# Kernel optimization log

Hardware: AMD Instinct MI355X
Metric: run time of the kernel (lower is better)

The kernel has to match this reference:

```python
import jax, jax.numpy as jnp
import numpy as np

B, H, W, C = 4, 48, 48, 256
NUM_HEADS = 8
DEPTH = C // NUM_HEADS  # 32


def setup_inputs() -> dict:
    key = jax.random.key(0)
    ks = jax.random.split(key, 8)
    scale = 1.0 / np.sqrt(C)
    return {
        "inputs": jax.random.normal(ks[0], (B, H, W, C), dtype=jnp.float32),
        "wq": jax.random.normal(ks[1], (C, C), dtype=jnp.float32) * scale,
        "bq": jax.random.normal(ks[2], (C,), dtype=jnp.float32) * 0.01,
        "wk": jax.random.normal(ks[3], (C, C), dtype=jnp.float32) * scale,
        "bk": jax.random.normal(ks[4], (C,), dtype=jnp.float32) * 0.01,
        "wv": jax.random.normal(ks[5], (C, C), dtype=jnp.float32) * scale,
        "bv": jax.random.normal(ks[6], (C,), dtype=jnp.float32) * 0.01,
        "gamma": jax.random.normal(ks[7], (), dtype=jnp.float32) * 0.1,
    }


def reference(inputs, wq, bq, wk, bk, wv, bv, gamma):
    b, h, w, c = inputs.shape
    n = h * w  # number of tokens

    def proj_split(wm, bm):
        # 1x1 conv == per-pixel dense: [b,h,w,c] @ [c,c] + bias
        y = jnp.einsum('bhwc,cd->bhwd', inputs, wm) + bm
        # split heads -> [b, num_heads, n, depth]
        return y.reshape(b, n, NUM_HEADS, DEPTH).transpose(0, 2, 1, 3)

    q = proj_split(wq, bq) / jnp.sqrt(jnp.asarray(DEPTH, inputs.dtype))
    k = proj_split(wk, bk)
    v = proj_split(wv, bv)

    s = jnp.einsum('bnqd,bnkd->bnqk', q, k)        # [b, heads, n, n]
    a = jax.nn.softmax(s, axis=-1)
    o = jnp.einsum('bnqk,bnkd->bnqd', a, v)        # [b, heads, n, depth]
    o = o.transpose(0, 2, 1, 3).reshape(b, h, w, c)
    return gamma * o + inputs
```

## Files before the change

kernel.cpp:

```cpp
#include <hip/hip_runtime.h>
#include <hip/hip_bf16.h>
#include <cstdint>

#define B_    4
#define NH    8
#define N_TOK 2304
#define D_    32
#define C_    256
#define M_ROWS (B_ * N_TOK)
#define KVB   128
#define NT2   (N_TOK / KVB)
#define M_FIX 10.0f

typedef float  f32x4  __attribute__((ext_vector_type(4)));
typedef short  bf16x8 __attribute__((ext_vector_type(8)));

#define GLOADLDS(g, l) __builtin_amdgcn_global_load_lds( \
    (const __attribute__((address_space(1))) unsigned*)(g), \
    (__attribute__((address_space(3))) unsigned*)(l), 16, 0, 0)

static __device__ __forceinline__ unsigned short f2bf(float f) {
    union { float f; unsigned u; } v; v.f = f;
    unsigned u = v.u;
    u += 0x7FFF + ((u >> 16) & 1);
    return (unsigned short)(u >> 16);
}

static __device__ __forceinline__ unsigned cvt_pk_bf16(float a, float b) {
    unsigned r;
    asm("v_cvt_pk_bf16_f32 %0, %1, %2" : "=v"(r) : "v"(a), "v"(b));
    return r;
}

__global__ void k_prep_x(const float* __restrict__ x, unsigned short* __restrict__ xb) {
    int i = blockIdx.x * blockDim.x + threadIdx.x;
    float4 v = reinterpret_cast<const float4*>(x)[i];
    ushort4 o;
    o.x = f2bf(v.x); o.y = f2bf(v.y); o.z = f2bf(v.z); o.w = f2bf(v.w);
    reinterpret_cast<ushort4*>(xb)[i] = o;
}

__global__ void k_prep_w(const float* __restrict__ w0, const float* __restrict__ w1,
                         const float* __restrict__ w2, unsigned short* __restrict__ wt) {
    __shared__ float tile[64][65];
    int mat = blockIdx.y;
    const float* w = (mat == 0) ? w0 : (mat == 1) ? w1 : w2;
    int t   = blockIdx.x;
    int tc  = (t & 3) * 64;
    int td  = (t >> 2) * 64;
    int tid = threadIdx.x;
    int r0  = tid >> 6;
    int x0  = tid & 63;
#pragma unroll
    for (int it = 0; it < 16; ++it) {
        int c = it * 4 + r0;
        tile[c][x0] = w[(tc + c) * C_ + td + x0];
    }
    __syncthreads();
    unsigned short* wto = wt + mat * (C_ * C_);
#pragma unroll
    for (int it = 0; it < 16; ++it) {
        int d = it * 4 + r0;
        wto[(td + d) * C_ + tc + x0] = f2bf(tile[x0][d]);
    }
}

__global__ __launch_bounds__(256) void k_proj(
    const unsigned short* __restrict__ xb,
    const unsigned short* __restrict__ wtb,
    const float* __restrict__ bq, const float* __restrict__ bk, const float* __restrict__ bv,
    unsigned short* __restrict__ qo, unsigned short* __restrict__ ko, unsigned short* __restrict__ vto)
{
    __shared__ __align__(16) unsigned short A_lds[2][64][32];
    __shared__ __align__(16) unsigned short B_lds[2][128][32];

    int rows0 = blockIdx.x * 64;
    int cols0 = blockIdx.y * 128;
    int mat   = cols0 >> 8;
    const float* bias = (mat == 0) ? bq : (mat == 1) ? bk : bv;
    float scale = (mat == 0) ? (0.17677669529663687f * 1.4426950408889634f) : 1.0f;

    int tid = threadIdx.x, wave = tid >> 6, lane = tid & 63;
    int lr = lane & 15, lg = lane >> 4;
    int wr = wave >> 1, wc = wave & 1;

    int srow = lane >> 2, sslot = lane & 3;
    int ra   = wave * 16 + srow;
    int keyA = ((ra >> 1) & 1) | (((ra >> 3) & 1) << 1);
    const unsigned short* asrc = xb + (rows0 + ra) * C_ + ((sslot ^ keyA) * 8);
    int rb   = wave * 32 + srow;
    int keyB0 = ((rb >> 1) & 1) | (((rb >> 3) & 1) << 1);
    int keyB1 = (((rb + 16) >> 1) & 1) | ((((rb + 16) >> 3) & 1) << 1);
    const unsigned short* bsrc0 = wtb + (cols0 + rb) * C_ + ((sslot ^ keyB0) * 8);
    const unsigned short* bsrc1 = wtb + (cols0 + rb + 16) * C_ + ((sslot ^ keyB1) * 8);

    char* aldsb = (char*)&A_lds[0][0][0];
    char* bldsb = (char*)&B_lds[0][0][0];
    int adst = wave * 1024;
    int bdst0 = wave * 2048, bdst1 = bdst0 + 1024;

    int xorb = (((lr >> 1) & 1) << 4) | (((lr >> 3) & 1) << 5);
    int fcol = (lg * 16) ^ xorb;
    int arow0 = wr * 32 + lr;
    int brow0 = wc * 64 + lr;

    GLOADLDS(asrc, aldsb + adst);
    GLOADLDS(bsrc0, bldsb + bdst0);
    GLOADLDS(bsrc1, bldsb + bdst1);
    __syncthreads();

    f32x4 acc[2][4];
#pragma unroll
    for (int i = 0; i < 2; ++i)
#pragma unroll
        for (int j = 0; j < 4; ++j) acc[i][j] = (f32x4){0.f, 0.f, 0.f, 0.f};

    int buf = 0;
    for (int ks = 0; ks < 8; ++ks) {
        if (ks < 7) {
            int ko_ = (ks + 1) * 32;
            char* ad = aldsb + (buf ^ 1) * 4096;
            char* bd = bldsb + (buf ^ 1) * 8192;
            GLOADLDS(asrc + ko_, ad + adst);
            GLOADLDS(bsrc0 + ko_, bd + bdst0);
            GLOADLDS(bsrc1 + ko_, bd + bdst1);
        }
        const char* ac = aldsb + buf * 4096;
        const char* bc = bldsb + buf * 8192;

        bf16x8 a[2], b[4];
#pragma unroll
        for (int fr = 0; fr < 2; ++fr)
            a[fr] = *reinterpret_cast<const bf16x8*>(ac + (arow0 + fr * 16) * 64 + fcol);
#pragma unroll
        for (int fn = 0; fn < 4; ++fn)
            b[fn] = *reinterpret_cast<const bf16x8*>(bc + (brow0 + fn * 16) * 64 + fcol);

        __builtin_amdgcn_s_setprio(1);
#pragma unroll
        for (int fr = 0; fr < 2; ++fr)
#pragma unroll
            for (int fn = 0; fn < 4; ++fn)
                acc[fr][fn] = __builtin_amdgcn_mfma_f32_16x16x32_bf16(a[fr], b[fn], acc[fr][fn], 0, 0, 0);
        __builtin_amdgcn_s_setprio(0);

        __syncthreads();
        buf ^= 1;
    }

    int bidx = rows0 / N_TOK;
    int nb   = rows0 - bidx * N_TOK + wr * 32 + lg * 4;

    if (mat == 2) {
#pragma unroll
        for (int fr = 0; fr < 2; ++fr)
#pragma unroll
            for (int fn = 0; fn < 4; ++fn) {
                int cm = (cols0 & 255) + wc * 64 + fn * 16 + lr;
                float bsv = bias[cm];
                int hh = cm >> 5, d = cm & 31;
                uint2 pr;
                pr.x = cvt_pk_bf16(acc[fr][fn][0] + bsv, acc[fr][fn][1] + bsv);
                pr.y = cvt_pk_bf16(acc[fr][fn][2] + bsv, acc[fr][fn][3] + bsv);
                *reinterpret_cast<uint2*>(vto + ((bidx * NH + hh) * D_ + d) * N_TOK + nb + fr * 16) = pr;
            }
    } else {
        unsigned short* dst = (mat == 0) ? qo : ko;
#pragma unroll
        for (int fr = 0; fr < 2; ++fr)
#pragma unroll
            for (int fn = 0; fn < 4; ++fn) {
                int cm = (cols0 & 255) + wc * 64 + fn * 16 + lr;
                float bsv = bias[cm];
                int hh = cm >> 5, d = cm & 31;
#pragma unroll
                for (int j = 0; j < 4; ++j) {
                    float val = (acc[fr][fn][j] + bsv) * scale;
                    dst[((bidx * NH + hh) * N_TOK + nb + fr * 16 + j) * D_ + d] = f2bf(val);
                }
            }
    }
}

__global__ __launch_bounds__(512, 4) void k_attn(
    const unsigned short* __restrict__ qb,
    const unsigned short* __restrict__ kb,
    const unsigned short* __restrict__ vtg,
    const float* __restrict__ x,
    const float* __restrict__ gamma_p,
    float* __restrict__ out)
{
    __shared__ __align__(16) unsigned short K_lds[3][KVB][32];
    __shared__ __align__(16) unsigned short Vt_lds[3][32][KVB];

    int wid = (blockIdx.x & 7) * 72 + (blockIdx.x >> 3);
    int bh  = wid / 18;
    int qb0 = (wid % 18) * 128;

    int tid = threadIdx.x, wave = tid >> 6, lane = tid & 63;
    int lr = lane & 15, lg = lane >> 4;

    const unsigned short* Q  = qb  + bh * N_TOK * D_;
    const unsigned short* K  = kb  + bh * N_TOK * D_;
    const unsigned short* Vt = vtg + bh * D_ * N_TOK;

    int qrow = qb0 + wave * 16 + lr;
    bf16x8 q_frag = *reinterpret_cast<const bf16x8*>(Q + qrow * D_ + lg * 8);

    bool stK = wave < 4;
    int  sw  = stK ? wave : (wave - 4);
    int c0   = sw * 2;
    int kr0  = 32 * sw + (lane >> 2);
    int kslot = ((kr0 >> 1) & 1) | (((kr0 >> 3) & 1) << 1);
    int koff0 = kr0 * D_ + (((lane & 3) ^ kslot) * 8);
    int koff1 = koff0 + 16 * D_;
    int vr0   = 8 * sw + (lane >> 4);
    int voff0 = vr0 * N_TOK + (((lane & 15) ^ (vr0 & 7)) * 8);
    int voff1 = (vr0 + 4) * N_TOK + (((lane & 15) ^ ((vr0 + 4) & 7)) * 8);

    char* kldsb = (char*)&K_lds[0][0][0];
    char* vldsb = (char*)&Vt_lds[0][0][0];
    int dst0 = c0 * 1024, dst1 = dst0 + 1024;

#define STAGE(st, bidx) do {                                    \
        if (stK) {                                              \
            const unsigned short* Kn = K + (st) * (KVB * D_);   \
            char* kd = kldsb + (bidx) * 8192;                   \
            GLOADLDS(Kn + koff0, kd + dst0);                    \
            GLOADLDS(Kn + koff1, kd + dst1);                    \
        } else {                                                \
            const unsigned short* Vn = Vt + (st) * KVB;         \
            char* vd = vldsb + (bidx) * 8192;                   \
            GLOADLDS(Vn + voff0, vd + dst0);                    \
            GLOADLDS(Vn + voff1, vd + dst1);                    \
        } } while (0)

    STAGE(0, 0);
    STAGE(1, 1);
    asm volatile("s_waitcnt vmcnt(2)" ::: "memory");
    __builtin_amdgcn_s_barrier();

    f32x4 acc0  = (f32x4){0.f, 0.f, 0.f, 0.f};
    f32x4 acc1  = (f32x4){0.f, 0.f, 0.f, 0.f};
    f32x4 acc_l = (f32x4){0.f, 0.f, 0.f, 0.f};

    union { unsigned w[4]; bf16x8 v; } ones;
    ones.w[0] = 0x3F803F80u; ones.w[1] = 0x3F803F80u;
    ones.w[2] = 0x3F803F80u; ones.w[3] = 0x3F803F80u;

    int kread_key = (((lr >> 1) & 1) << 4) | (((lr >> 2) & 1) << 5);
    int krow_lane = (8 * (lr >> 2) + (lr & 3)) * 64 + ((lg * 16) ^ kread_key);
    int vkey = (lr & 7) << 4;

    const f32x4 zinit = (f32x4){-M_FIX, -M_FIX, -M_FIX, -M_FIX};

    int b0 = 0;
    for (int t = 0; t < NT2; ++t) {
        if (t + 2 < NT2) {
            int b2 = b0 + 2; if (b2 >= 3) b2 -= 3;
            STAGE(t + 2, b2);
        }
        const char* kc = kldsb + b0 * 8192;
        const char* vc = vldsb + b0 * 8192;

        f32x4 s[8];
        __builtin_amdgcn_s_setprio(1);
#pragma unroll
        for (int kt = 0; kt < 8; ++kt) {
            bf16x8 kf = *reinterpret_cast<const bf16x8*>(
                kc + (kt >> 1) * 2048 + (kt & 1) * 256 + krow_lane);
            s[kt] = __builtin_amdgcn_mfma_f32_16x16x32_bf16(kf, q_frag, zinit, 0, 0, 0);
        }
        __builtin_amdgcn_s_setprio(0);

#pragma unroll
        for (int kseg = 0; kseg < 4; ++kseg) {
            float e0 = __builtin_amdgcn_exp2f(s[2 * kseg][0]);
            float e1 = __builtin_amdgcn_exp2f(s[2 * kseg][1]);
            float e2 = __builtin_amdgcn_exp2f(s[2 * kseg][2]);
            float e3 = __builtin_amdgcn_exp2f(s[2 * kseg][3]);
            float e4 = __builtin_amdgcn_exp2f(s[2 * kseg + 1][0]);
            float e5 = __builtin_amdgcn_exp2f(s[2 * kseg + 1][1]);
            float e6 = __builtin_amdgcn_exp2f(s[2 * kseg + 1][2]);
            float e7 = __builtin_amdgcn_exp2f(s[2 * kseg + 1][3]);
            union { unsigned w[4]; bf16x8 v; } pa;
            pa.w[0] = cvt_pk_bf16(e0, e1);
            pa.w[1] = cvt_pk_bf16(e2, e3);
            pa.w[2] = cvt_pk_bf16(e4, e5);
            pa.w[3] = cvt_pk_bf16(e6, e7);
            int off = (kseg * 64 + lg * 16) ^ vkey;
            bf16x8 vf0 = *reinterpret_cast<const bf16x8*>(vc + lr * 256 + off);
            bf16x8 vf1 = *reinterpret_cast<const bf16x8*>(vc + (16 + lr) * 256 + off);
            acc0  = __builtin_amdgcn_mfma_f32_16x16x32_bf16(pa.v, vf0,    acc0,  0, 0, 0);
            acc1  = __builtin_amdgcn_mfma_f32_16x16x32_bf16(pa.v, vf1,    acc1,  0, 0, 0);
            acc_l = __builtin_amdgcn_mfma_f32_16x16x32_bf16(pa.v, ones.v, acc_l, 0, 0, 0);
        }

        if (t < NT2 - 1) {
            if (t + 2 < NT2) asm volatile("s_waitcnt vmcnt(2)" ::: "memory");
            else             asm volatile("s_waitcnt vmcnt(0)" ::: "memory");
            __builtin_amdgcn_s_barrier();
        }
        b0 = (b0 + 1 == 3) ? 0 : b0 + 1;
    }
#undef STAGE

    float g = gamma_p[0];
    int b = bh >> 3, head = bh & 7;
#pragma unroll
    for (int j = 0; j < 4; ++j) {
        float linv = 1.0f / acc_l[j];
        int n = qb0 + wave * 16 + 4 * lg + j;
        long r = (long)(b * N_TOK + n) * C_ + head * 32;
        out[r + lr]      = g * (acc0[j] * linv) + x[r + lr];
        out[r + 16 + lr] = g * (acc1[j] * linv) + x[r + 16 + lr];
    }
}

extern "C" void kernel_launch(void* const* d_in, const int* in_sizes, int n_in,
                              void* d_out, int out_size, void* d_ws, size_t ws_size,
                              hipStream_t stream) {
    const float* x     = (const float*)d_in[0];
    const float* wq    = (const float*)d_in[1];
    const float* bq    = (const float*)d_in[2];
    const float* wk    = (const float*)d_in[3];
    const float* bk    = (const float*)d_in[4];
    const float* wv    = (const float*)d_in[5];
    const float* bv    = (const float*)d_in[6];
    const float* gamma = (const float*)d_in[7];
    float* out = (float*)d_out;

    char* ws = (char*)d_ws;
    unsigned short* xb   = (unsigned short*)(ws);
    unsigned short* wt   = (unsigned short*)(ws + 4718592);
    unsigned short* qbuf = (unsigned short*)(ws + 5111808);
    unsigned short* kbuf = (unsigned short*)(ws + 9830400);
    unsigned short* vtg  = (unsigned short*)(ws + 14548992);

    k_prep_x<<<dim3(M_ROWS * C_ / 1024), dim3(256), 0, stream>>>(x, xb);
    k_prep_w<<<dim3(16, 3), dim3(256), 0, stream>>>(wq, wk, wv, wt);
    k_proj<<<dim3(M_ROWS / 64, 6), dim3(256), 0, stream>>>(xb, wt, bq, bk, bv, qbuf, kbuf, vtg);
    k_attn<<<dim3(N_TOK / 128 * B_ * NH), dim3(512), 0, stream>>>(qbuf, kbuf, vtg, x, gamma, out);
}
```

Measured before the change: 62.81 us.

## Triple-buffer projection GEMM loads and shrink attention blocks to six waves

The projection kernel moves from double to triple-buffered LDS staging, prefetching two k-steps ahead and using explicit vmcnt waits instead of a full syncthreads. The attention kernel now uses 384-thread blocks covering 96 query rows instead of 128. Four waves stage K and two waves stage V with four loads each, and the grid grows to 768 blocks. The aim is better latency hiding in the GEMM and better CU load balance in attention. The cost is more LDS per projection block and more redundant K/V loads per query row.

```diff
diff --git a/kernel.cpp b/kernel.cpp
--- a/kernel.cpp
+++ b/kernel.cpp
@@ -71,8 +71,8 @@
     const float* __restrict__ bq, const float* __restrict__ bk, const float* __restrict__ bv,
     unsigned short* __restrict__ qo, unsigned short* __restrict__ ko, unsigned short* __restrict__ vto)
 {
-    __shared__ __align__(16) unsigned short A_lds[2][64][32];
-    __shared__ __align__(16) unsigned short B_lds[2][128][32];
+    __shared__ __align__(16) unsigned short A_lds[3][64][32];
+    __shared__ __align__(16) unsigned short B_lds[3][128][32];
 
     int rows0 = blockIdx.x * 64;
     int cols0 = blockIdx.y * 128;
@@ -104,10 +104,19 @@
     int arow0 = wr * 32 + lr;
     int brow0 = wc * 64 + lr;
 
-    GLOADLDS(asrc, aldsb + adst);
-    GLOADLDS(bsrc0, bldsb + bdst0);
-    GLOADLDS(bsrc1, bldsb + bdst1);
-    __syncthreads();
+#define PSTAGE(ks, bidx) do {                               \
+        int ko_ = (ks) * 32;                                \
+        char* ad = aldsb + (bidx) * 4096;                   \
+        char* bd = bldsb + (bidx) * 8192;                   \
+        GLOADLDS(asrc + ko_, ad + adst);                    \
+        GLOADLDS(bsrc0 + ko_, bd + bdst0);                  \
+        GLOADLDS(bsrc1 + ko_, bd + bdst1);                  \
+    } while (0)
+
+    PSTAGE(0, 0);
+    PSTAGE(1, 1);
+    asm volatile("s_waitcnt vmcnt(3)" ::: "memory");
+    __builtin_amdgcn_s_barrier();
 
     f32x4 acc[2][4];
 #pragma unroll
@@ -115,18 +124,14 @@
 #pragma unroll
         for (int j = 0; j < 4; ++j) acc[i][j] = (f32x4){0.f, 0.f, 0.f, 0.f};
 
-    int buf = 0;
+    int b0 = 0;
     for (int ks = 0; ks < 8; ++ks) {
-        if (ks < 7) {
-            int ko_ = (ks + 1) * 32;
-            char* ad = aldsb + (buf ^ 1) * 4096;
-            char* bd = bldsb + (buf ^ 1) * 8192;
-            GLOADLDS(asrc + ko_, ad + adst);
-            GLOADLDS(bsrc0 + ko_, bd + bdst0);
-            GLOADLDS(bsrc1 + ko_, bd + bdst1);
-        }
-        const char* ac = aldsb + buf * 4096;
-        const char* bc = bldsb + buf * 8192;
+        if (ks + 2 < 8) {
+            int b2 = b0 + 2; if (b2 >= 3) b2 -= 3;
+            PSTAGE(ks + 2, b2);
+        }
+        const char* ac = aldsb + b0 * 4096;
+        const char* bc = bldsb + b0 * 8192;
 
         bf16x8 a[2], b[4];
 #pragma unroll
@@ -144,9 +149,14 @@
                 acc[fr][fn] = __builtin_amdgcn_mfma_f32_16x16x32_bf16(a[fr], b[fn], acc[fr][fn], 0, 0, 0);
         __builtin_amdgcn_s_setprio(0);
 
-        __syncthreads();
-        buf ^= 1;
-    }
+        if (ks < 7) {
+            if (ks + 2 < 8) asm volatile("s_waitcnt vmcnt(3)" ::: "memory");
+            else            asm volatile("s_waitcnt vmcnt(0)" ::: "memory");
+            __builtin_amdgcn_s_barrier();
+        }
+        b0 = (b0 + 1 == 3) ? 0 : b0 + 1;
+    }
+#undef PSTAGE
 
     int bidx = rows0 / N_TOK;
     int nb   = rows0 - bidx * N_TOK + wr * 32 + lg * 4;
@@ -182,7 +192,7 @@
     }
 }
 
-__global__ __launch_bounds__(512, 4) void k_attn(
+__global__ __launch_bounds__(384, 4) void k_attn(
     const unsigned short* __restrict__ qb,
     const unsigned short* __restrict__ kb,
     const unsigned short* __restrict__ vtg,
@@ -193,9 +203,9 @@
     __shared__ __align__(16) unsigned short K_lds[3][KVB][32];
     __shared__ __align__(16) unsigned short Vt_lds[3][32][KVB];
 
-    int wid = (blockIdx.x & 7) * 72 + (blockIdx.x >> 3);
-    int bh  = wid / 18;
-    int qb0 = (wid % 18) * 128;
+    int wid = (blockIdx.x & 7) * 96 + (blockIdx.x >> 3);
+    int bh  = wid / 24;
+    int qb0 = (wid % 24) * 96;
 
     int tid = threadIdx.x, wave = tid >> 6, lane = tid & 63;
     int lr = lane & 15, lg = lane >> 4;
@@ -208,36 +218,50 @@
     bf16x8 q_frag = *reinterpret_cast<const bf16x8*>(Q + qrow * D_ + lg * 8);
 
     bool stK = wave < 4;
-    int  sw  = stK ? wave : (wave - 4);
-    int c0   = sw * 2;
-    int kr0  = 32 * sw + (lane >> 2);
+    int kr0  = 32 * wave + (lane >> 2);
     int kslot = ((kr0 >> 1) & 1) | (((kr0 >> 3) & 1) << 1);
     int koff0 = kr0 * D_ + (((lane & 3) ^ kslot) * 8);
     int koff1 = koff0 + 16 * D_;
-    int vr0   = 8 * sw + (lane >> 4);
-    int voff0 = vr0 * N_TOK + (((lane & 15) ^ (vr0 & 7)) * 8);
-    int voff1 = (vr0 + 4) * N_TOK + (((lane & 15) ^ ((vr0 + 4) & 7)) * 8);
+    int kdst0 = wave * 2048 + lane * 16;
+    int kdst1 = kdst0 + 1024;
+    int vw    = wave - 4;
+    int vbase = 16 * vw + (lane >> 4);
+    int c8    = lane & 15;
+    int voffA = (vbase)      * N_TOK + ((c8 ^ ((vbase)      & 7)) * 8);
+    int voffB = (vbase + 4)  * N_TOK + ((c8 ^ ((vbase + 4)  & 7)) * 8);
+    int voffC = (vbase + 8)  * N_TOK + ((c8 ^ ((vbase + 8)  & 7)) * 8);
+    int voffD = (vbase + 12) * N_TOK + ((c8 ^ ((vbase + 12) & 7)) * 8);
+    int vdstA = (4 * vw + 0) * 1024 + lane * 16;
+    int vdstB = vdstA + 1024;
+    int vdstC = vdstA + 2048;
+    int vdstD = vdstA + 3072;
 
     char* kldsb = (char*)&K_lds[0][0][0];
     char* vldsb = (char*)&Vt_lds[0][0][0];
-    int dst0 = c0 * 1024, dst1 = dst0 + 1024;
 
 #define STAGE(st, bidx) do {                                    \
         if (stK) {                                              \
             const unsigned short* Kn = K + (st) * (KVB * D_);   \
             char* kd = kldsb + (bidx) * 8192;                   \
-            GLOADLDS(Kn + koff0, kd + dst0);                    \
-            GLOADLDS(Kn + koff1, kd + dst1);                    \
+            GLOADLDS(Kn + koff0, kd + kdst0);                   \
+            GLOADLDS(Kn + koff1, kd + kdst1);                   \
         } else {                                                \
             const unsigned short* Vn = Vt + (st) * KVB;         \
             char* vd = vldsb + (bidx) * 8192;                   \
-            GLOADLDS(Vn + voff0, vd + dst0);                    \
-            GLOADLDS(Vn + voff1, vd + dst1);                    \
+            GLOADLDS(Vn + voffA, vd + vdstA);                   \
+            GLOADLDS(Vn + voffB, vd + vdstB);                   \
+            GLOADLDS(Vn + voffC, vd + vdstC);                   \
+            GLOADLDS(Vn + voffD, vd + vdstD);                   \
         } } while (0)
+
+#define WAIT_PREV() do {                                        \
+        if (stK) asm volatile("s_waitcnt vmcnt(2)" ::: "memory"); \
+        else     asm volatile("s_waitcnt vmcnt(4)" ::: "memory"); \
+    } while (0)
 
     STAGE(0, 0);
     STAGE(1, 1);
-    asm volatile("s_waitcnt vmcnt(2)" ::: "memory");
+    WAIT_PREV();
     __builtin_amdgcn_s_barrier();
 
     f32x4 acc0  = (f32x4){0.f, 0.f, 0.f, 0.f};
@@ -297,13 +321,14 @@
         }
 
         if (t < NT2 - 1) {
-            if (t + 2 < NT2) asm volatile("s_waitcnt vmcnt(2)" ::: "memory");
+            if (t + 2 < NT2) WAIT_PREV();
             else             asm volatile("s_waitcnt vmcnt(0)" ::: "memory");
             __builtin_amdgcn_s_barrier();
         }
         b0 = (b0 + 1 == 3) ? 0 : b0 + 1;
     }
 #undef STAGE
+#undef WAIT_PREV
 
     float g = gamma_p[0];
     int b = bh >> 3, head = bh & 7;
@@ -340,5 +365,5 @@
     k_prep_x<<<dim3(M_ROWS * C_ / 1024), dim3(256), 0, stream>>>(x, xb);
     k_prep_w<<<dim3(16, 3), dim3(256), 0, stream>>>(wq, wk, wv, wt);
     k_proj<<<dim3(M_ROWS / 64, 6), dim3(256), 0, stream>>>(xb, wt, bq, bk, bv, qbuf, kbuf, vtg);
-    k_attn<<<dim3(N_TOK / 128 * B_ * NH), dim3(512), 0, stream>>>(qbuf, kbuf, vtg, x, gamma, out);
-}
+    k_attn<<<dim3(N_TOK / 96 * B_ * NH), dim3(384), 0, stream>>>(qbuf, kbuf, vtg, x, gamma, out);
+}
```

New measurement: 68.03 us. +8.3%, slower.
